# Kernel optimization log

Hardware: AMD Instinct MI355X
Metric: run time of the kernel (lower is better)

Reference implementation:

```python
import jax, jax.numpy as jnp
import numpy as np

MAX_SHIFT = 64  # init kwarg; alpha=None -> score_max branch


def setup_inputs() -> dict:
    key = jax.random.key(0)
    k1, k2 = jax.random.split(key)
    x = jax.random.normal(k1, (64, 2, 4096), dtype=jnp.float32)
    y = jax.random.normal(k2, (64, 2, 4096), dtype=jnp.float32)
    return {"x": x, "y": y}


def reference(x, y):
    S = MAX_SHIFT
    W = 2 * S + 1  # num_windows
    # forward(): flip along channel axis
    x = jnp.flip(x, axis=1)
    B, C, D = x.shape
    # min-max normalize each (batch, channel) trace to [-1, 1]
    xmin = x.min(axis=-1, keepdims=True)
    xmax = x.max(axis=-1, keepdims=True)
    x = 2 * (x - xmin) / (xmax - xmin) - 1
    # torch.hann_window(dim) is periodic: 0.5*(1 - cos(2*pi*n/N))
    hann = 0.5 * (1.0 - jnp.cos(2.0 * jnp.pi * jnp.arange(D, dtype=x.dtype) / D))
    x = x * hann
    # pad by max_shift on both sides, then take W sliding windows of length D
    xpad = jnp.pad(x, ((0, 0), (0, 0), (S, S)))  # [B, C, D+2S]
    idx = jnp.arange(W)[:, None] + jnp.arange(D)[None, :]  # [W, D]
    xw = xpad[:, :, idx]  # [B, C, W, D] (matches torch unfold+reshape)
    xw = jnp.transpose(xw, (2, 0, 1, 3))  # [W, B, C, D]
    # mean-centered Pearson correlation per window
    xc = xw - xw.mean(axis=-1, keepdims=True)
    yc = y - y.mean(axis=-1, keepdims=True)
    corr = jnp.sum(xc * yc, axis=-1)  # [W, B, C]
    norm = jnp.sum(xc * xc, axis=-1) * jnp.sum(yc * yc, axis=-1)
    corr = corr / jnp.sqrt(norm)
    # alpha is None -> score_max: max over shifts, L2 over channels
    values = corr.max(axis=0)  # [B, C]
    scores = jnp.sqrt(jnp.sum(values ** 2, axis=-1))  # [B]
    return -scores.mean()
```

## Files before the change

kernel.cpp:

```cpp
#include <hip/hip_runtime.h>
#include <math.h>

#define DD      4096
#define WW      129
#define XSN     4240
#define NP      4
#define BLOCKN  256

__global__ __launch_bounds__(BLOCKN) void spl_main(
        const float* __restrict__ x, const float* __restrict__ y,
        float* __restrict__ partial) {
    const int blk = blockIdx.x;
    const int bc  = blk >> 2, p = blk & 3;
    const int b   = bc >> 1,  c = bc & 1;
    const float* xp = x + (size_t)(b * 2 + (1 - c)) * DD;
    const float* yp = y + (size_t)(b * 2 + c) * DD;
    const float4* xp4 = (const float4*)xp;
    const float4* yp4 = (const float4*)yp;

    __shared__ __align__(16) float xs[XSN];
    __shared__ float P0s[65], P0q[65], Qs[65], Qq[65];
    __shared__ float red[20];
    __shared__ float wred[4];

    const int tid = threadIdx.x, lane = tid & 63, wv = tid >> 6;

    if (tid < 36) {
        int i4 = (tid < 16) ? tid : (1024 + tid);
        ((float4*)xs)[i4] = make_float4(0.f, 0.f, 0.f, 0.f);
    }

    float xmn = 3.0e38f, xmx = -3.0e38f, ysum = 0.0f;
    #pragma unroll
    for (int it = 0; it < 4; ++it) {
        float4 xv = xp4[tid + 256 * it];
        float4 yv = yp4[tid + 256 * it];
        xmn = fminf(xmn, fminf(fminf(xv.x, xv.y), fminf(xv.z, xv.w)));
        xmx = fmaxf(xmx, fmaxf(fmaxf(xv.x, xv.y), fmaxf(xv.z, xv.w)));
        ysum += (yv.x + yv.y) + (yv.z + yv.w);
    }
    #pragma unroll
    for (int off = 32; off > 0; off >>= 1) {
        xmn  = fminf(xmn, __shfl_down(xmn, off, 64));
        xmx  = fmaxf(xmx, __shfl_down(xmx, off, 64));
        ysum += __shfl_down(ysum, off, 64);
    }
    if (lane == 0) { red[wv] = xmn; red[4 + wv] = xmx; red[8 + wv] = ysum; }
    __syncthreads();
    xmn = fminf(fminf(red[0], red[1]), fminf(red[2], red[3]));
    xmx = fmaxf(fmaxf(red[4], red[5]), fmaxf(red[6], red[7]));
    const float ymean = (red[8] + red[9] + red[10] + red[11]) * (1.0f / (float)DD);
    const float a   = 2.0f / (xmx - xmn);
    const float bsh = -a * xmn - 1.0f;

    float ssum = 0.0f, ssq = 0.0f;
    #pragma unroll
    for (int it = 0; it < 4; ++it) {
        int i4 = tid + 256 * it;
        float4 xv = xp4[i4];
        float fd = (float)(4 * i4);
        float4 h;
        h.x = 0.5f - 0.5f * __builtin_amdgcn_cosf((fd + 0.0f) * (1.0f / (float)DD));
        h.y = 0.5f - 0.5f * __builtin_amdgcn_cosf((fd + 1.0f) * (1.0f / (float)DD));
        h.z = 0.5f - 0.5f * __builtin_amdgcn_cosf((fd + 2.0f) * (1.0f / (float)DD));
        h.w = 0.5f - 0.5f * __builtin_amdgcn_cosf((fd + 3.0f) * (1.0f / (float)DD));
        float4 v;
        v.x = fmaf(a, xv.x, bsh) * h.x;
        v.y = fmaf(a, xv.y, bsh) * h.y;
        v.z = fmaf(a, xv.z, bsh) * h.z;
        v.w = fmaf(a, xv.w, bsh) * h.w;
        ((float4*)(xs + 64))[i4] = v;
        ssum += (v.x + v.y) + (v.z + v.w);
        ssq = fmaf(v.x, v.x, fmaf(v.y, v.y, fmaf(v.z, v.z, fmaf(v.w, v.w, ssq))));
    }

    float4 yc4[16];
    float syy = 0.0f;
    #pragma unroll
    for (int i = 0; i < 16; ++i) {
        float4 v = yp4[64 * i + lane];
        v.x -= ymean; v.y -= ymean; v.z -= ymean; v.w -= ymean;
        yc4[i] = v;
        syy = fmaf(v.x, v.x, fmaf(v.y, v.y, fmaf(v.z, v.z, fmaf(v.w, v.w, syy))));
    }
    #pragma unroll
    for (int off = 32; off > 0; off >>= 1) {
        ssum += __shfl_down(ssum, off, 64);
        ssq  += __shfl_down(ssq,  off, 64);
        syy  += __shfl_down(syy,  off, 64);
    }
    if (lane == 0) { red[12 + wv] = ssum; red[16 + wv] = ssq; }
    syy = __shfl(syy, 0, 64);

    if (wv == 0) {
        int d = lane;
        float h = 0.5f - 0.5f * __builtin_amdgcn_cosf((float)d * (1.0f / (float)DD));
        float v = fmaf(a, xp[d], bsh) * h;
        float s = v, sq = v * v;
        #pragma unroll
        for (int off = 1; off < 64; off <<= 1) {
            float t  = __shfl_up(s,  off, 64);
            float tq = __shfl_up(sq, off, 64);
            if (lane >= off) { s += t; sq += tq; }
        }
        P0s[lane + 1] = s; P0q[lane + 1] = sq;
        if (lane == 0) { P0s[0] = 0.0f; P0q[0] = 0.0f; }
    } else if (wv == 1) {
        int d = 4032 + lane;
        float h = 0.5f - 0.5f * __builtin_amdgcn_cosf((float)d * (1.0f / (float)DD));
        float v = fmaf(a, xp[d], bsh) * h;
        float s = v, sq = v * v;
        #pragma unroll
        for (int off = 1; off < 64; off <<= 1) {
            float t  = __shfl_up(s,  off, 64);
            float tq = __shfl_up(sq, off, 64);
            if (lane >= off) { s += t; sq += tq; }
        }
        float Ts = __shfl(s, 63, 64), Tq = __shfl(sq, 63, 64);
        Qs[lane] = Ts - (s - v);
        Qq[lane] = Tq - (sq - v * v);
        if (lane == 63) { Qs[64] = 0.0f; Qq[64] = 0.0f; }
    }
    __syncthreads();
    const float Stot  = (red[12] + red[13]) + (red[14] + red[15]);
    const float Sqtot = (red[16] + red[17]) + (red[18] + red[19]);

    const float4* xs4 = (const float4*)xs;
    float vmax = -3.0e38f;
    for (int g = p + 4 * wv; g <= 16; g += 16) {
        float cr[8];
        #pragma unroll
        for (int j = 0; j < 8; ++j) cr[j] = 0.0f;
        const int A0 = lane + 2 * g;
        #pragma unroll
        for (int i = 0; i < 16; ++i) {
            int A = 64 * i + A0;
            float4 x0 = xs4[A], x1 = xs4[A + 1], x2 = xs4[A + 2];
            float wnd[12] = { x0.x, x0.y, x0.z, x0.w,
                              x1.x, x1.y, x1.z, x1.w,
                              x2.x, x2.y, x2.z, x2.w };
            float4 yv = yc4[i];
            #pragma unroll
            for (int j = 0; j < 8; ++j)
                cr[j] = fmaf(yv.x, wnd[j],
                        fmaf(yv.y, wnd[j + 1],
                        fmaf(yv.z, wnd[j + 2],
                        fmaf(yv.w, wnd[j + 3], cr[j]))));
        }
        #pragma unroll
        for (int off = 32; off > 0; off >>= 1) {
            #pragma unroll
            for (int j = 0; j < 8; ++j) cr[j] += __shfl_down(cr[j], off, 64);
        }
        if (lane == 0) {
            #pragma unroll
            for (int j = 0; j < 8; ++j) {
                int w = 8 * g + j;
                if (w < WW) {
                    int hidx = (w > 64) ? (w - 64) : 0;
                    int tidx = (w < 64) ? w : 64;
                    float sx   = Stot  - P0s[hidx] - Qs[tidx];
                    float sxx  = Sqtot - P0q[hidx] - Qq[tidx];
                    float varx = sxx - sx * sx * (1.0f / (float)DD);
                    float corr = cr[j] / sqrtf(varx * syy);
                    vmax = fmaxf(vmax, corr);
                }
            }
        }
    }
    if (lane == 0) wred[wv] = vmax;
    __syncthreads();
    if (tid == 0)
        partial[blk] = fmaxf(fmaxf(wred[0], wred[1]), fmaxf(wred[2], wred[3]));
}

__global__ void spl_final(const float* __restrict__ partial,
                          float* __restrict__ out) {
    const int b = threadIdx.x;
    float v0 = -3.0e38f, v1 = -3.0e38f;
    #pragma unroll
    for (int pp = 0; pp < NP; ++pp) {
        v0 = fmaxf(v0, partial[(b * 2 + 0) * NP + pp]);
        v1 = fmaxf(v1, partial[(b * 2 + 1) * NP + pp]);
    }
    float s = sqrtf(v0 * v0 + v1 * v1);
    #pragma unroll
    for (int off = 32; off > 0; off >>= 1) s += __shfl_down(s, off, 64);
    if (b == 0) out[0] = -s * (1.0f / 64.0f);
}

extern "C" void kernel_launch(void* const* d_in, const int* in_sizes, int n_in,
                              void* d_out, int out_size, void* d_ws, size_t ws_size,
                              hipStream_t stream) {
    const float* x = (const float*)d_in[0];
    const float* y = (const float*)d_in[1];
    float* out     = (float*)d_out;
    float* partial = (float*)d_ws;

    spl_main<<<dim3(128 * NP), dim3(BLOCKN), 0, stream>>>(x, y, partial);
    spl_final<<<dim3(1), dim3(64), 0, stream>>>(partial, out);
}
```

Measured before the change: 69.75 us.

## Fuse final reduction into main kernel via last-block atomic counter

Replaces the separate single-block finalisation kernel with a last-block-done pattern: each block publishes its max into a device global and increments an atomic counter, and the last block performs the L2/mean reduction and resets the counter. It also issues all x and y global loads up front, computes the Hann window before the min/max reduction, and reuses the loaded y registers instead of reloading. This removes one kernel launch and the global round-trip between kernels, and gives more memory-level parallelism in the prologue. In exchange it adds atomic traffic and raises register pressure from keeping the x, y and window values live.

```diff
diff --git a/kernel.cpp b/kernel.cpp
--- a/kernel.cpp
+++ b/kernel.cpp
@@ -4,12 +4,15 @@
 #define DD      4096
 #define WW      129
 #define XSN     4240
-#define NP      4
 #define BLOCKN  256
-
-__global__ __launch_bounds__(BLOCKN) void spl_main(
+#define NBLK    512
+
+__device__ float g_part[NBLK];
+__device__ int   g_cnt = 0;
+
+__global__ __launch_bounds__(BLOCKN) void spl_fused(
         const float* __restrict__ x, const float* __restrict__ y,
-        float* __restrict__ partial) {
+        float* __restrict__ out) {
     const int blk = blockIdx.x;
     const int bc  = blk >> 2, p = blk & 3;
     const int b   = bc >> 1,  c = bc & 1;
@@ -20,8 +23,9 @@
 
     __shared__ __align__(16) float xs[XSN];
     __shared__ float P0s[65], P0q[65], Qs[65], Qq[65];
-    __shared__ float red[20];
+    __shared__ float red[16];
     __shared__ float wred[4];
+    __shared__ int lastFlag;
 
     const int tid = threadIdx.x, lane = tid & 63, wv = tid >> 6;
 
@@ -30,26 +34,52 @@
         ((float4*)xs)[i4] = make_float4(0.f, 0.f, 0.f, 0.f);
     }
 
-    float xmn = 3.0e38f, xmx = -3.0e38f, ysum = 0.0f;
+    float4 xv4[4];
+    #pragma unroll
+    for (int it = 0; it < 4; ++it) xv4[it] = xp4[tid + 256 * it];
+    float4 yv4[16];
+    #pragma unroll
+    for (int i = 0; i < 16; ++i) yv4[i] = yp4[64 * i + lane];
+
+    float4 h4[4];
     #pragma unroll
     for (int it = 0; it < 4; ++it) {
-        float4 xv = xp4[tid + 256 * it];
-        float4 yv = yp4[tid + 256 * it];
+        float fd = (float)(4 * (tid + 256 * it));
+        h4[it].x = 0.5f - 0.5f * __builtin_amdgcn_cosf((fd + 0.0f) * (1.0f / (float)DD));
+        h4[it].y = 0.5f - 0.5f * __builtin_amdgcn_cosf((fd + 1.0f) * (1.0f / (float)DD));
+        h4[it].z = 0.5f - 0.5f * __builtin_amdgcn_cosf((fd + 2.0f) * (1.0f / (float)DD));
+        h4[it].w = 0.5f - 0.5f * __builtin_amdgcn_cosf((fd + 3.0f) * (1.0f / (float)DD));
+    }
+
+    float xmn = 3.0e38f, xmx = -3.0e38f;
+    #pragma unroll
+    for (int it = 0; it < 4; ++it) {
+        float4 xv = xv4[it];
         xmn = fminf(xmn, fminf(fminf(xv.x, xv.y), fminf(xv.z, xv.w)));
         xmx = fmaxf(xmx, fmaxf(fmaxf(xv.x, xv.y), fmaxf(xv.z, xv.w)));
-        ysum += (yv.x + yv.y) + (yv.z + yv.w);
     }
     #pragma unroll
     for (int off = 32; off > 0; off >>= 1) {
-        xmn  = fminf(xmn, __shfl_down(xmn, off, 64));
-        xmx  = fmaxf(xmx, __shfl_down(xmx, off, 64));
-        ysum += __shfl_down(ysum, off, 64);
-    }
-    if (lane == 0) { red[wv] = xmn; red[4 + wv] = xmx; red[8 + wv] = ysum; }
+        xmn = fminf(xmn, __shfl_down(xmn, off, 64));
+        xmx = fmaxf(xmx, __shfl_down(xmx, off, 64));
+    }
+    if (lane == 0) { red[wv] = xmn; red[4 + wv] = xmx; }
+
+    float ys0 = 0.0f, ys1 = 0.0f;
+    #pragma unroll
+    for (int i = 0; i < 16; i += 2) {
+        ys0 += (yv4[i].x + yv4[i].y) + (yv4[i].z + yv4[i].w);
+        ys1 += (yv4[i + 1].x + yv4[i + 1].y) + (yv4[i + 1].z + yv4[i + 1].w);
+    }
+    float ysum = ys0 + ys1;
+    #pragma unroll
+    for (int off = 32; off > 0; off >>= 1) ysum += __shfl_down(ysum, off, 64);
+    ysum = __shfl(ysum, 0, 64);
+    const float ymean = ysum * (1.0f / (float)DD);
+
     __syncthreads();
     xmn = fminf(fminf(red[0], red[1]), fminf(red[2], red[3]));
     xmx = fmaxf(fmaxf(red[4], red[5]), fmaxf(red[6], red[7]));
-    const float ymean = (red[8] + red[9] + red[10] + red[11]) * (1.0f / (float)DD);
     const float a   = 2.0f / (xmx - xmn);
     const float bsh = -a * xmn - 1.0f;
 
@@ -57,39 +87,33 @@
     #pragma unroll
     for (int it = 0; it < 4; ++it) {
         int i4 = tid + 256 * it;
-        float4 xv = xp4[i4];
-        float fd = (float)(4 * i4);
-        float4 h;
-        h.x = 0.5f - 0.5f * __builtin_amdgcn_cosf((fd + 0.0f) * (1.0f / (float)DD));
-        h.y = 0.5f - 0.5f * __builtin_amdgcn_cosf((fd + 1.0f) * (1.0f / (float)DD));
-        h.z = 0.5f - 0.5f * __builtin_amdgcn_cosf((fd + 2.0f) * (1.0f / (float)DD));
-        h.w = 0.5f - 0.5f * __builtin_amdgcn_cosf((fd + 3.0f) * (1.0f / (float)DD));
         float4 v;
-        v.x = fmaf(a, xv.x, bsh) * h.x;
-        v.y = fmaf(a, xv.y, bsh) * h.y;
-        v.z = fmaf(a, xv.z, bsh) * h.z;
-        v.w = fmaf(a, xv.w, bsh) * h.w;
+        v.x = fmaf(a, xv4[it].x, bsh) * h4[it].x;
+        v.y = fmaf(a, xv4[it].y, bsh) * h4[it].y;
+        v.z = fmaf(a, xv4[it].z, bsh) * h4[it].z;
+        v.w = fmaf(a, xv4[it].w, bsh) * h4[it].w;
         ((float4*)(xs + 64))[i4] = v;
         ssum += (v.x + v.y) + (v.z + v.w);
         ssq = fmaf(v.x, v.x, fmaf(v.y, v.y, fmaf(v.z, v.z, fmaf(v.w, v.w, ssq))));
     }
-
-    float4 yc4[16];
-    float syy = 0.0f;
-    #pragma unroll
-    for (int i = 0; i < 16; ++i) {
-        float4 v = yp4[64 * i + lane];
-        v.x -= ymean; v.y -= ymean; v.z -= ymean; v.w -= ymean;
-        yc4[i] = v;
-        syy = fmaf(v.x, v.x, fmaf(v.y, v.y, fmaf(v.z, v.z, fmaf(v.w, v.w, syy))));
-    }
     #pragma unroll
     for (int off = 32; off > 0; off >>= 1) {
         ssum += __shfl_down(ssum, off, 64);
         ssq  += __shfl_down(ssq,  off, 64);
-        syy  += __shfl_down(syy,  off, 64);
-    }
-    if (lane == 0) { red[12 + wv] = ssum; red[16 + wv] = ssq; }
+    }
+    if (lane == 0) { red[8 + wv] = ssum; red[12 + wv] = ssq; }
+
+    float sy0 = 0.0f, sy1 = 0.0f;
+    #pragma unroll
+    for (int i = 0; i < 16; ++i) {
+        yv4[i].x -= ymean; yv4[i].y -= ymean; yv4[i].z -= ymean; yv4[i].w -= ymean;
+        float* acc = (i & 1) ? &sy1 : &sy0;
+        *acc = fmaf(yv4[i].x, yv4[i].x, fmaf(yv4[i].y, yv4[i].y,
+               fmaf(yv4[i].z, yv4[i].z, fmaf(yv4[i].w, yv4[i].w, *acc))));
+    }
+    float syy = sy0 + sy1;
+    #pragma unroll
+    for (int off = 32; off > 0; off >>= 1) syy += __shfl_down(syy, off, 64);
     syy = __shfl(syy, 0, 64);
 
     if (wv == 0) {
@@ -122,8 +146,8 @@
         if (lane == 63) { Qs[64] = 0.0f; Qq[64] = 0.0f; }
     }
     __syncthreads();
-    const float Stot  = (red[12] + red[13]) + (red[14] + red[15]);
-    const float Sqtot = (red[16] + red[17]) + (red[18] + red[19]);
+    const float Stot  = (red[8]  + red[9])  + (red[10] + red[11]);
+    const float Sqtot = (red[12] + red[13]) + (red[14] + red[15]);
 
     const float4* xs4 = (const float4*)xs;
     float vmax = -3.0e38f;
@@ -139,7 +163,7 @@
             float wnd[12] = { x0.x, x0.y, x0.z, x0.w,
                               x1.x, x1.y, x1.z, x1.w,
                               x2.x, x2.y, x2.z, x2.w };
-            float4 yv = yc4[i];
+            float4 yv = yv4[i];
             #pragma unroll
             for (int j = 0; j < 8; ++j)
                 cr[j] = fmaf(yv.x, wnd[j],
@@ -170,23 +194,35 @@
     }
     if (lane == 0) wred[wv] = vmax;
     __syncthreads();
-    if (tid == 0)
-        partial[blk] = fmaxf(fmaxf(wred[0], wred[1]), fmaxf(wred[2], wred[3]));
-}
-
-__global__ void spl_final(const float* __restrict__ partial,
-                          float* __restrict__ out) {
-    const int b = threadIdx.x;
-    float v0 = -3.0e38f, v1 = -3.0e38f;
-    #pragma unroll
-    for (int pp = 0; pp < NP; ++pp) {
-        v0 = fmaxf(v0, partial[(b * 2 + 0) * NP + pp]);
-        v1 = fmaxf(v1, partial[(b * 2 + 1) * NP + pp]);
-    }
-    float s = sqrtf(v0 * v0 + v1 * v1);
-    #pragma unroll
-    for (int off = 32; off > 0; off >>= 1) s += __shfl_down(s, off, 64);
-    if (b == 0) out[0] = -s * (1.0f / 64.0f);
+
+    if (tid == 0) {
+        float bm = fmaxf(fmaxf(wred[0], wred[1]), fmaxf(wred[2], wred[3]));
+        __hip_atomic_store(&g_part[blk], bm, __ATOMIC_RELEASE,
+                           __HIP_MEMORY_SCOPE_AGENT);
+        int old = __hip_atomic_fetch_add(&g_cnt, 1, __ATOMIC_ACQ_REL,
+                                         __HIP_MEMORY_SCOPE_AGENT);
+        lastFlag = (old == NBLK - 1) ? 1 : 0;
+    }
+    __syncthreads();
+    if (lastFlag != 0 && wv == 0) {
+        const int bb = lane;
+        float v0 = -3.0e38f, v1 = -3.0e38f;
+        #pragma unroll
+        for (int pp = 0; pp < 4; ++pp) {
+            v0 = fmaxf(v0, __hip_atomic_load(&g_part[(bb * 2 + 0) * 4 + pp],
+                            __ATOMIC_RELAXED, __HIP_MEMORY_SCOPE_AGENT));
+            v1 = fmaxf(v1, __hip_atomic_load(&g_part[(bb * 2 + 1) * 4 + pp],
+                            __ATOMIC_RELAXED, __HIP_MEMORY_SCOPE_AGENT));
+        }
+        float s = sqrtf(v0 * v0 + v1 * v1);
+        #pragma unroll
+        for (int off = 32; off > 0; off >>= 1) s += __shfl_down(s, off, 64);
+        if (lane == 0) {
+            out[0] = -s * (1.0f / 64.0f);
+            __hip_atomic_store(&g_cnt, 0, __ATOMIC_RELAXED,
+                               __HIP_MEMORY_SCOPE_AGENT);
+        }
+    }
 }
 
 extern "C" void kernel_launch(void* const* d_in, const int* in_sizes, int n_in,
@@ -195,8 +231,7 @@
     const float* x = (const float*)d_in[0];
     const float* y = (const float*)d_in[1];
     float* out     = (float*)d_out;
-    float* partial = (float*)d_ws;
-
-    spl_main<<<dim3(128 * NP), dim3(BLOCKN), 0, stream>>>(x, y, partial);
-    spl_final<<<dim3(1), dim3(64), 0, stream>>>(partial, out);
+    (void)d_ws; (void)ws_size;
+
+    spl_fused<<<dim3(NBLK), dim3(BLOCKN), 0, stream>>>(x, y, out);
 }
```

After: 77.72 us. 1.11x slower.
